# Performance work log

Measured on AMD Instinct MI355X. Metric: run time of the kernel, lower is better.

The kernel has to match this reference:

```python
import jax, jax.numpy as jnp
import numpy as np

N_NODES = 100000
N_EDGES = 3200000
F_IN = 16
F_HID = 32


def _gcn_conv(x, row, col, edge_w, W, b, num_nodes):
    # PyG GCNConv: gcn_norm with add_self_loops=True (fill_value=1.0),
    # symmetric normalization, then x @ W.T aggregated over edges, + bias.
    loop = jnp.arange(num_nodes)
    r = jnp.concatenate([row, loop])
    c = jnp.concatenate([col, loop])
    ew = jnp.concatenate([edge_w, jnp.ones((num_nodes,), dtype=edge_w.dtype)])
    deg = jax.ops.segment_sum(ew, c, num_segments=num_nodes)
    dis = jnp.where(deg > 0, jax.lax.rsqrt(deg), 0.0)
    norm = dis[r] * ew * dis[c]  # [E+N]
    xw = x @ W.T                 # [N, out]
    msg = xw[r] * norm[:, None]  # gather + scale
    out = jax.ops.segment_sum(msg, c, num_segments=num_nodes)
    return out + b


def setup_inputs() -> dict:
    key = jax.random.key(0)
    ks = jax.random.split(key, 8)
    x = jax.random.normal(ks[0], (N_NODES, F_IN), dtype=jnp.float32)
    edge_index = jax.random.randint(ks[1], (2, N_EDGES), 0, N_NODES, dtype=jnp.int64)
    edge_w = jax.random.uniform(ks[2], (N_EDGES,), dtype=jnp.float32)
    W1 = jax.random.normal(ks[3], (F_HID, F_IN), dtype=jnp.float32) * 0.1
    b1 = jax.random.normal(ks[4], (F_HID,), dtype=jnp.float32) * 0.1
    W2 = jax.random.normal(ks[5], (F_IN, F_HID), dtype=jnp.float32) * 0.1
    b2 = jax.random.normal(ks[6], (F_IN,), dtype=jnp.float32) * 0.1
    return {"x": x, "edge_index": edge_index, "edge_w": edge_w,
            "W1": W1, "b1": b1, "W2": W2, "b2": b2, "num_nodes": N_NODES}


def reference(x, edge_index, edge_w, W1, b1, W2, b2, num_nodes):
    row, col = edge_index[0], edge_index[1]
    h = _gcn_conv(x, row, col, edge_w, W1, b1, num_nodes)
    h = jax.nn.relu(h)
    out = _gcn_conv(h, row, col, edge_w, W2, b2, num_nodes)
    return out
```

## Files before the change

kernel.cpp:

```cpp
#include <hip/hip_runtime.h>
#include <hip/hip_fp16.h>
#include <cstdint>


#define BS 256
#define CHUNKS 256
#define GNODES 16
#define GCAP 2048

__device__ __forceinline__ int2 nt_load_edge(const int2* p) {
    long long v = __builtin_nontemporal_load((const long long*)p);
    int2 r;
    r.x = (int)(v & 0xFFFFFFFFll);
    r.y = (int)(v >> 32);
    return r;
}

__device__ __forceinline__ float4 load_h4(const __half* p) {
    uint2 u = *(const uint2*)p;
    __half2 p0 = *(__half2*)&u.x;
    __half2 p1 = *(__half2*)&u.y;
    float2 f0 = __half22float2(p0);
    float2 f1 = __half22float2(p1);
    float4 r;
    r.x = f0.x; r.y = f0.y; r.z = f1.x; r.w = f1.y;
    return r;
}

__global__ __launch_bounds__(1024) void hist_kernel(
        const int* __restrict__ col, int* __restrict__ part,
        int E, int nbuck, int per) {
    extern __shared__ int sh[];
    for (int t = threadIdx.x; t < nbuck; t += blockDim.x) sh[t] = 0;
    __syncthreads();
    int lo = blockIdx.x * per, hi = min(E, lo + per);
    for (int e = lo + threadIdx.x; e < hi; e += blockDim.x)
        atomicAdd(&sh[col[e] >> 8], 1);
    __syncthreads();
    for (int t = threadIdx.x; t < nbuck; t += blockDim.x)
        part[(size_t)blockIdx.x * nbuck + t] = sh[t];
}

__global__ void colscan_kernel(const int* __restrict__ part, int* __restrict__ base,
                               int* __restrict__ tot, int nbuck) {
    int b = blockIdx.x;
    if (b >= nbuck) return;
    int lane = threadIdx.x;
    int off = 0;
    for (int g = 0; g < CHUNKS; g += 64) {
        int c = g + lane;
        int v = part[(size_t)c * nbuck + b];
        int s = v;
        #pragma unroll
        for (int d = 1; d < 64; d <<= 1) {
            int t = __shfl_up(s, d);
            if (lane >= d) s += t;
        }
        base[(size_t)c * nbuck + b] = off + (s - v);
        off += __shfl(s, 63);
    }
    if (lane == 0) tot[b] = off;
}

__global__ void scan1_kernel(const int* __restrict__ cnt, int* __restrict__ excl,
                             int* __restrict__ bsum, int n) {
    __shared__ int s[256];
    int tid = threadIdx.x;
    int i = blockIdx.x * 256 + tid;
    int v = (i < n) ? cnt[i] : 0;
    s[tid] = v;
    __syncthreads();
    for (int off = 1; off < 256; off <<= 1) {
        int t = (tid >= off) ? s[tid - off] : 0;
        __syncthreads();
        s[tid] += t;
        __syncthreads();
    }
    if (i < n) excl[i] = s[tid] - v;
    if (tid == 255) bsum[blockIdx.x] = s[255];
}

__global__ void scan2_kernel(int* __restrict__ bsum, int nb) {
    __shared__ int s[512];
    int tid = threadIdx.x;
    int v = (tid < nb) ? bsum[tid] : 0;
    s[tid] = v;
    __syncthreads();
    for (int off = 1; off < 512; off <<= 1) {
        int t = (tid >= off) ? s[tid - off] : 0;
        __syncthreads();
        s[tid] += t;
        __syncthreads();
    }
    if (tid < nb) bsum[tid] = s[tid] - v;
}

__global__ void scan3_kernel(int* __restrict__ excl, const int* __restrict__ bsum,
                             int n, int E) {
    int i = blockIdx.x * 256 + threadIdx.x;
    if (i < n) excl[i] += bsum[i >> 8];
    else if (i == n) excl[n] = E;
}

__global__ __launch_bounds__(1024) void place_kernel(
        const int* __restrict__ row, const int* __restrict__ col,
        const float* __restrict__ ew,
        const int* __restrict__ start, const int* __restrict__ base,
        int2* __restrict__ rw, int E, int nbuck, int per) {
    extern __shared__ int sh[];
    int* lbase = sh;
    int* cnt2  = sh + nbuck;
    int c = blockIdx.x;
    for (int t = threadIdx.x; t < nbuck; t += blockDim.x) {
        lbase[t] = start[t] + base[(size_t)c * nbuck + t];
        cnt2[t] = 0;
    }
    __syncthreads();
    int lo = c * per, hi = min(E, lo + per);
    for (int e = lo + threadIdx.x; e < hi; e += blockDim.x) {
        int cc = col[e];
        int b = cc >> 8;
        int p = lbase[b] + atomicAdd(&cnt2[b], 1);
        int2 v;
        v.x = row[e] | ((cc & 255) << 20);
        v.y = __float_as_int(ew[e]);
        rw[p] = v;
    }
}

__global__ __launch_bounds__(512) void nodesort_kernel(
        const int2* __restrict__ rw, const int* __restrict__ start,
        int2* __restrict__ rw2, int* __restrict__ ptr,
        float* __restrict__ dis, int N, int E, int nbuck) {
    __shared__ int cnt[BS];
    __shared__ float fdeg[BS];
    __shared__ int fill[BS];
    __shared__ int stmp[BS];
    int b = blockIdx.x, tid = threadIdx.x;
    for (int t = tid; t < BS; t += 512) { cnt[t] = 0; fdeg[t] = 0.f; }
    __syncthreads();
    int s0 = start[b], s1 = start[b + 1];
    for (int e = s0 + tid; e < s1; e += 512) {
        int2 v = rw[e];
        int cl = v.x >> 20;
        atomicAdd(&cnt[cl], 1);
        atomicAdd(&fdeg[cl], __int_as_float(v.y));
    }
    __syncthreads();

    int myc = 0;
    if (tid < BS) { myc = cnt[tid]; stmp[tid] = myc; }
    __syncthreads();
    for (int off = 1; off < BS; off <<= 1) {
        int t = 0;
        if (tid < BS && tid >= off) t = stmp[tid - off];
        __syncthreads();
        if (tid < BS) stmp[tid] += t;
        __syncthreads();
    }
    if (tid < BS) {
        int excl = stmp[tid] - myc;
        ptr[b * BS + tid] = s0 + excl;
        fill[tid] = excl;
        int node = b * BS + tid;
        if (node < N) dis[node] = rsqrtf(fdeg[tid] + 1.0f);
    }
    __syncthreads();

    for (int e = s0 + tid; e < s1; e += 512) {
        int2 v = rw[e];
        int cl = v.x >> 20;
        int p = s0 + atomicAdd(&fill[cl], 1);
        int2 o;
        o.x = v.x & 0xFFFFF;
        o.y = v.y;
        rw2[p] = o;
    }
    if (b == 0 && tid == 0) ptr[nbuck * BS] = E;
}

__global__ void xsc_kernel(const float* __restrict__ x, const float* __restrict__ dis,
                           __half* __restrict__ xsc, int N) {
    int i = blockIdx.x * 256 + threadIdx.x;
    if (i >= N) return;
    float d = dis[i];
    const float4* xr = (const float4*)(x + (size_t)i * 16);
    __half2 h[8];
#pragma unroll
    for (int k = 0; k < 4; ++k) {
        float4 v = xr[k];
        h[2*k]   = __floats2half2_rn(v.x * d, v.y * d);
        h[2*k+1] = __floats2half2_rn(v.z * d, v.w * d);
    }
    uint4* dst = (uint4*)(xsc + (size_t)i * 16);
    dst[0] = *(uint4*)&h[0];
    dst[1] = *(uint4*)&h[4];
}

template <int FINAL>
__global__ __launch_bounds__(1024) void gather_kernel(
        const int* __restrict__ ptr, const int2* __restrict__ rw2,
        const __half* __restrict__ src, const float* __restrict__ dis,
        const float* __restrict__ b2, float* __restrict__ dst, int N) {
    __shared__ int2 se[GCAP];
    __shared__ int sptr[GNODES + 1];
    int tid = threadIdx.x;
    int base = blockIdx.x * GNODES;
    if (tid <= GNODES) sptr[tid] = ptr[base + tid];
    __syncthreads();
    int w0 = sptr[0];
    int count = min(sptr[GNODES] - w0, GCAP);
    for (int i = tid; i < count; i += 1024)
        se[i] = nt_load_edge(&rw2[w0 + i]);
    __syncthreads();

    int wave = tid >> 6;
    int node = base + wave;
    if (node >= N) return;
    int lane = tid & 63;
    int slot = lane >> 2;
    int q    = lane & 3;
    int s0 = sptr[wave], s1 = sptr[wave + 1];

    float4 a0 = {0.f, 0.f, 0.f, 0.f}, a1 = {0.f, 0.f, 0.f, 0.f};
    int e = s0 + slot;
    for (; e + 16 < s1; e += 32) {
        int li0 = e - w0, li1 = li0 + 16;
        int2 v0 = (li0 < GCAP) ? se[li0] : nt_load_edge(&rw2[e]);
        int2 v1 = (li1 < GCAP) ? se[li1] : nt_load_edge(&rw2[e + 16]);
        float4 x0 = load_h4(src + (size_t)v0.x * 16 + q * 4);
        float4 x1 = load_h4(src + (size_t)v1.x * 16 + q * 4);
        float w0f = __int_as_float(v0.y), w1f = __int_as_float(v1.y);
        a0.x += w0f * x0.x; a0.y += w0f * x0.y; a0.z += w0f * x0.z; a0.w += w0f * x0.w;
        a1.x += w1f * x1.x; a1.y += w1f * x1.y; a1.z += w1f * x1.z; a1.w += w1f * x1.w;
    }
    if (e < s1) {
        int li = e - w0;
        int2 v0 = (li < GCAP) ? se[li] : nt_load_edge(&rw2[e]);
        float4 x0 = load_h4(src + (size_t)v0.x * 16 + q * 4);
        float w0f = __int_as_float(v0.y);
        a0.x += w0f * x0.x; a0.y += w0f * x0.y; a0.z += w0f * x0.z; a0.w += w0f * x0.w;
    }
    a0.x += a1.x; a0.y += a1.y; a0.z += a1.z; a0.w += a1.w;
#pragma unroll
    for (int m = 4; m <= 32; m <<= 1) {
        a0.x += __shfl_xor(a0.x, m);
        a0.y += __shfl_xor(a0.y, m);
        a0.z += __shfl_xor(a0.z, m);
        a0.w += __shfl_xor(a0.w, m);
    }

    if (slot == 0) {
        float d = dis[node];
        float4 self = load_h4(src + (size_t)node * 16 + q * 4);
        float4 o;
        o.x = d * (a0.x + self.x);
        o.y = d * (a0.y + self.y);
        o.z = d * (a0.z + self.z);
        o.w = d * (a0.w + self.w);
        if (FINAL) {
            float4 bb = *(const float4*)(b2 + q * 4);
            o.x += bb.x; o.y += bb.y; o.z += bb.z; o.w += bb.w;
        }
        *(float4*)(dst + (size_t)node * 16 + q * 4) = o;
    }
}

__global__ __launch_bounds__(256) void mlp_kernel(
        const float* __restrict__ t, const float* __restrict__ dis,
        const float* __restrict__ W1, const float* __restrict__ b1,
        const float* __restrict__ W2, __half* __restrict__ xs2, int N) {
    __shared__ float sW1[512];
    __shared__ float sW2[512];
    __shared__ float sb1[32];
    for (int k = threadIdx.x; k < 512; k += 256) {
        sW1[k] = W1[k];
        sW2[k] = W2[k];
    }
    if (threadIdx.x < 32) sb1[threadIdx.x] = b1[threadIdx.x];
    __syncthreads();
    int i = blockIdx.x * 256 + threadIdx.x;
    if (i >= N) return;

    float tr[16];
#pragma unroll
    for (int k = 0; k < 4; ++k) {
        float4 v = ((const float4*)(t + (size_t)i * 16))[k];
        tr[4*k+0] = v.x; tr[4*k+1] = v.y; tr[4*k+2] = v.z; tr[4*k+3] = v.w;
    }
    float h[32];
#pragma unroll
    for (int o = 0; o < 32; ++o) {
        float acc = sb1[o];
#pragma unroll
        for (int k = 0; k < 16; ++k) acc += tr[k] * sW1[o * 16 + k];
        h[o] = fmaxf(acc, 0.f);
    }
    float d = dis[i];
    float o16[16];
#pragma unroll
    for (int o = 0; o < 16; ++o) {
        float acc = 0.f;
#pragma unroll
        for (int k = 0; k < 32; ++k) acc += h[k] * sW2[o * 32 + k];
        o16[o] = acc * d;
    }
    __half2 hh[8];
#pragma unroll
    for (int k = 0; k < 8; ++k) hh[k] = __floats2half2_rn(o16[2*k], o16[2*k+1]);
    uint4* dst = (uint4*)(xs2 + (size_t)i * 16);
    dst[0] = *(uint4*)&hh[0];
    dst[1] = *(uint4*)&hh[4];
}


extern "C" void kernel_launch(void* const* d_in, const int* in_sizes, int n_in,
                              void* d_out, int out_size, void* d_ws, size_t ws_size,
                              hipStream_t stream) {
    const float* x  = (const float*)d_in[0];
    const int*   ei = (const int*)d_in[1];
    const float* ew = (const float*)d_in[2];
    const float* W1 = (const float*)d_in[3];
    const float* b1 = (const float*)d_in[4];
    const float* W2 = (const float*)d_in[5];
    const float* b2 = (const float*)d_in[6];
    float* out = (float*)d_out;

    const int N = in_sizes[0] / 16;
    const int E = in_sizes[2];
    const int* row = ei;
    const int* col = ei + E;

    const int nbuck = (N + BS - 1) / BS;
    const int per   = (E + CHUNKS - 1) / CHUNKS;
    const int nb    = (nbuck + 255) / 256;

    float*  ws    = (float*)d_ws;
    int2*   rw2   = (int2*)ws;
    int2*   rw    = (int2*)(ws + (size_t)2 * E);
    __half* xsc   = (__half*)(ws + (size_t)2 * E);
    float*  tbuf  = ws + (size_t)2 * E + (size_t)8 * N;
    __half* xs2   = (__half*)(ws + (size_t)2 * E + (size_t)24 * N);
    float*  dis   = ws + (size_t)4 * E;
    int*    ptr   = (int*)(dis + N);
    int*    part  = ptr + (size_t)BS * nbuck + 1;
    int*    base  = part + (size_t)CHUNKS * nbuck;
    int*    tot   = base + (size_t)CHUNKS * nbuck;
    int*    start = tot + nbuck;
    int*    bsum  = start + nbuck + 1;

    hist_kernel<<<CHUNKS, 1024, nbuck * 4, stream>>>(col, part, E, nbuck, per);
    colscan_kernel<<<nbuck, 64, 0, stream>>>(part, base, tot, nbuck);
    scan1_kernel<<<nb, 256, 0, stream>>>(tot, start, bsum, nbuck);
    scan2_kernel<<<1, 512, 0, stream>>>(bsum, nb);
    scan3_kernel<<<(nbuck + 256) / 256 + 1, 256, 0, stream>>>(start, bsum, nbuck, E);
    place_kernel<<<CHUNKS, 1024, 2 * nbuck * 4, stream>>>(row, col, ew, start, base, rw, E, nbuck, per);
    nodesort_kernel<<<nbuck, 512, 0, stream>>>(rw, start, rw2, ptr, dis, N, E, nbuck);

    xsc_kernel<<<(N + 255) / 256, 256, 0, stream>>>(x, dis, xsc, N);
    {
        int gblocks = (N + GNODES - 1) / GNODES;
        gather_kernel<0><<<gblocks, 1024, 0, stream>>>(ptr, rw2, xsc, dis, b2, tbuf, N);
        mlp_kernel<<<(N + 255) / 256, 256, 0, stream>>>(tbuf, dis, W1, b1, W2, xs2, N);
        gather_kernel<1><<<gblocks, 1024, 0, stream>>>(ptr, rw2, xs2, dis, b2, out, N);
    }
}
```

Baseline: 191.1 us.

## Map four nodes per wave in gather and drop LDS edge staging

The gather kernel now assigns 16 lanes per destination node (4 nodes per wavefront) instead of a full wave per node, and uses 256-thread blocks without shared-memory staging of the edge list. Edge source indices are pre-shifted by 5 in nodesort so they serve directly as byte offsets into the half-precision feature table, which saves an address multiply. With an average of about 32 edges per node, a whole wave per node left many lanes idle and needed deep shuffle reductions. The new mapping cuts lane waste and syncthreads, but every edge is now loaded straight from global memory and nodes of very different degree in one wave can diverge.

```diff
diff --git a/kernel.cpp b/kernel.cpp
--- a/kernel.cpp
+++ b/kernel.cpp
@@ -5,8 +5,6 @@
 
 #define BS 256
 #define CHUNKS 256
-#define GNODES 16
-#define GCAP 2048
 
 __device__ __forceinline__ int2 nt_load_edge(const int2* p) {
     long long v = __builtin_nontemporal_load((const long long*)p);
@@ -172,7 +170,7 @@
         int cl = v.x >> 20;
         int p = s0 + atomicAdd(&fill[cl], 1);
         int2 o;
-        o.x = v.x & 0xFFFFF;
+        o.x = (v.x & 0xFFFFF) << 5;
         o.y = v.y;
         rw2[p] = o;
     }
@@ -198,61 +196,50 @@
 }
 
 template <int FINAL>
-__global__ __launch_bounds__(1024) void gather_kernel(
+__global__ __launch_bounds__(256) void gather_kernel(
         const int* __restrict__ ptr, const int2* __restrict__ rw2,
         const __half* __restrict__ src, const float* __restrict__ dis,
         const float* __restrict__ b2, float* __restrict__ dst, int N) {
-    __shared__ int2 se[GCAP];
-    __shared__ int sptr[GNODES + 1];
-    int tid = threadIdx.x;
-    int base = blockIdx.x * GNODES;
-    if (tid <= GNODES) sptr[tid] = ptr[base + tid];
-    __syncthreads();
-    int w0 = sptr[0];
-    int count = min(sptr[GNODES] - w0, GCAP);
-    for (int i = tid; i < count; i += 1024)
-        se[i] = nt_load_edge(&rw2[w0 + i]);
-    __syncthreads();
-
+    int tid  = threadIdx.x;
     int wave = tid >> 6;
-    int node = base + wave;
+    int lane = tid & 63;
+    int g = lane >> 4;
+    int s = (lane >> 2) & 3;
+    int q = lane & 3;
+    int node = (blockIdx.x * 4 + wave) * 4 + g;
     if (node >= N) return;
-    int lane = tid & 63;
-    int slot = lane >> 2;
-    int q    = lane & 3;
-    int s0 = sptr[wave], s1 = sptr[wave + 1];
-
+    int s0 = ptr[node], s1 = ptr[node + 1];
+
+    const char* srcb = (const char*)src;
     float4 a0 = {0.f, 0.f, 0.f, 0.f}, a1 = {0.f, 0.f, 0.f, 0.f};
-    int e = s0 + slot;
-    for (; e + 16 < s1; e += 32) {
-        int li0 = e - w0, li1 = li0 + 16;
-        int2 v0 = (li0 < GCAP) ? se[li0] : nt_load_edge(&rw2[e]);
-        int2 v1 = (li1 < GCAP) ? se[li1] : nt_load_edge(&rw2[e + 16]);
-        float4 x0 = load_h4(src + (size_t)v0.x * 16 + q * 4);
-        float4 x1 = load_h4(src + (size_t)v1.x * 16 + q * 4);
-        float w0f = __int_as_float(v0.y), w1f = __int_as_float(v1.y);
-        a0.x += w0f * x0.x; a0.y += w0f * x0.y; a0.z += w0f * x0.z; a0.w += w0f * x0.w;
-        a1.x += w1f * x1.x; a1.y += w1f * x1.y; a1.z += w1f * x1.z; a1.w += w1f * x1.w;
+    int e = s0 + s;
+    for (; e + 4 < s1; e += 8) {
+        int2 v0 = nt_load_edge(&rw2[e]);
+        int2 v1 = nt_load_edge(&rw2[e + 4]);
+        float4 x0 = load_h4((const __half*)(srcb + v0.x) + q * 4);
+        float4 x1 = load_h4((const __half*)(srcb + v1.x) + q * 4);
+        float w0 = __int_as_float(v0.y), w1 = __int_as_float(v1.y);
+        a0.x += w0 * x0.x; a0.y += w0 * x0.y; a0.z += w0 * x0.z; a0.w += w0 * x0.w;
+        a1.x += w1 * x1.x; a1.y += w1 * x1.y; a1.z += w1 * x1.z; a1.w += w1 * x1.w;
     }
     if (e < s1) {
-        int li = e - w0;
-        int2 v0 = (li < GCAP) ? se[li] : nt_load_edge(&rw2[e]);
-        float4 x0 = load_h4(src + (size_t)v0.x * 16 + q * 4);
-        float w0f = __int_as_float(v0.y);
-        a0.x += w0f * x0.x; a0.y += w0f * x0.y; a0.z += w0f * x0.z; a0.w += w0f * x0.w;
+        int2 v0 = nt_load_edge(&rw2[e]);
+        float4 x0 = load_h4((const __half*)(srcb + v0.x) + q * 4);
+        float w0 = __int_as_float(v0.y);
+        a0.x += w0 * x0.x; a0.y += w0 * x0.y; a0.z += w0 * x0.z; a0.w += w0 * x0.w;
     }
     a0.x += a1.x; a0.y += a1.y; a0.z += a1.z; a0.w += a1.w;
 #pragma unroll
-    for (int m = 4; m <= 32; m <<= 1) {
+    for (int m = 4; m <= 8; m <<= 1) {
         a0.x += __shfl_xor(a0.x, m);
         a0.y += __shfl_xor(a0.y, m);
         a0.z += __shfl_xor(a0.z, m);
         a0.w += __shfl_xor(a0.w, m);
     }
 
-    if (slot == 0) {
+    if (s == 0) {
         float d = dis[node];
-        float4 self = load_h4(src + (size_t)node * 16 + q * 4);
+        float4 self = load_h4((const __half*)(srcb + ((size_t)node << 5)) + q * 4);
         float4 o;
         o.x = d * (a0.x + self.x);
         o.y = d * (a0.y + self.y);
@@ -312,7 +299,6 @@
     dst[0] = *(uint4*)&hh[0];
     dst[1] = *(uint4*)&hh[4];
 }
-
 
 extern "C" void kernel_launch(void* const* d_in, const int* in_sizes, int n_in,
                               void* d_out, int out_size, void* d_ws, size_t ws_size,
@@ -359,9 +345,9 @@
 
     xsc_kernel<<<(N + 255) / 256, 256, 0, stream>>>(x, dis, xsc, N);
     {
-        int gblocks = (N + GNODES - 1) / GNODES;
-        gather_kernel<0><<<gblocks, 1024, 0, stream>>>(ptr, rw2, xsc, dis, b2, tbuf, N);
+        int gblocks = (N + 15) / 16;
+        gather_kernel<0><<<gblocks, 256, 0, stream>>>(ptr, rw2, xsc, dis, b2, tbuf, N);
         mlp_kernel<<<(N + 255) / 256, 256, 0, stream>>>(tbuf, dis, W1, b1, W2, xs2, N);
-        gather_kernel<1><<<gblocks, 1024, 0, stream>>>(ptr, rw2, xs2, dis, b2, out, N);
-    }
-}
+        gather_kernel<1><<<gblocks, 256, 0, stream>>>(ptr, rw2, xs2, dis, b2, out, N);
+    }
+}
```

New measurement: 177.9 us. -6.9%, faster.
